# Kernel tuning notes

Hardware: AMD Instinct MI355X
Metric: run time of the kernel (lower is better)

## Reference

```python
import jax, jax.numpy as jnp
import numpy as np

TOP_K = 2
EPS = float(np.finfo(np.float64).eps)  # combine() clamps zeros to np.finfo(float).eps


def setup_inputs() -> dict:
    key = jax.random.key(0)
    ks = jax.random.split(key, 6)
    B, D, H, O, E = 2048, 1024, 2048, 512, 8
    return {
        "x": jax.random.normal(ks[0], (B, D), dtype=jnp.float32),
        "w_gate": jax.random.normal(ks[1], (D, E), dtype=jnp.float32) * 0.02,
        "fc1_w": jax.random.normal(ks[2], (E, D, H), dtype=jnp.float32) * 0.02,
        "fc1_b": jax.random.normal(ks[3], (E, H), dtype=jnp.float32) * 0.02,
        "fc2_w": jax.random.normal(ks[4], (E, H, O), dtype=jnp.float32) * 0.02,
        "fc2_b": jax.random.normal(ks[5], (E, O), dtype=jnp.float32) * 0.02,
    }


def _gates(x, w_gate):
    # Noisy top-k gating in eval mode (no noise): clean logits -> top-k -> softmax over top-k -> scatter.
    logits = x @ w_gate                              # [B, E]
    top_logits, top_idx = jax.lax.top_k(logits, TOP_K)  # [B, K]
    top_gates = jax.nn.softmax(top_logits, axis=-1)      # 'softmax' gating over selected experts
    B = x.shape[0]
    gates = jnp.zeros(logits.shape, logits.dtype)
    gates = gates.at[jnp.arange(B)[:, None], top_idx].set(top_gates)
    return gates                                      # [B, E], zero for non-selected experts


def reference(x, w_gate, fc1_w, fc1_b, fc2_w, fc2_b):
    gates = _gates(x, w_gate)                         # [B, E]
    # Dense-equivalent of SparseDispatcher: non-selected experts have gate 0,
    # so weighting by gates reproduces dispatch/expert/combine exactly.
    h = jax.nn.gelu(jnp.einsum('bd,edh->ebh', x, fc1_w) + fc1_b[:, None, :],
                    approximate=False)                # [E, B, H]
    logp = jax.nn.log_softmax(jnp.einsum('ebh,eho->ebo', h, fc2_w) + fc2_b[:, None, :],
                              axis=-1)                # [E, B, O] (MLP ends with LogSoftmax)
    # combine: sum_e gates[b,e] * exp(logp_e[b]), clamp zeros to eps, then log
    combined = jnp.einsum('ebo,be->bo', jnp.exp(logp), gates)  # [B, O]
    combined = jnp.where(combined == 0, jnp.asarray(EPS, combined.dtype), combined)
    return jnp.log(combined)
```

## Files before the change

kernel.cpp:

```cpp
#include <hip/hip_runtime.h>
#include <stdint.h>

#define Bn 2048
#define Dn 1024
#define Hn 2048
#define On 512
#define En 8

typedef __bf16 bf16x8 __attribute__((ext_vector_type(8)));
typedef float f32x4 __attribute__((ext_vector_type(4)));
typedef unsigned short ushort_t;
typedef ushort_t ushort4v __attribute__((ext_vector_type(4)));

__device__ __forceinline__ ushort_t f2bf(float v) {
  union { float f; uint32_t u; } a; a.f = v;
  uint32_t u = a.u;
  return (ushort_t)((u + 0x7fffu + ((u >> 16) & 1u)) >> 16);
}

__device__ __forceinline__ void gload16(const void* g, void* l) {
  __builtin_amdgcn_global_load_lds((const uint32_t*)g, (uint32_t*)l, 16, 0, 0);
}

__global__ void init_kernel(int* counts, int* cursors) {
  int t = threadIdx.x;
  if (t < En) { counts[t] = 0; cursors[t] = 0; }
}

#define NB_G (Bn / 8)
#define NB_T1 ((Dn / 64) * (Hn / 64) * En)
#define NB_T2 ((Hn / 64) * (On / 64) * En)

__device__ __forceinline__ void tcast64(const float* __restrict__ inp, ushort_t* __restrict__ outp,
                                        int R, int C, int r0, int c0, float* tile ) {
  int t = threadIdx.x;
  int rr = t >> 4;
  int cc4 = (t & 15) * 4;
#pragma unroll
  for (int j = 0; j < 4; j++) {
    float4 v = *(const float4*)&inp[(size_t)(r0 + j * 16 + rr) * C + c0 + cc4];
    float* tp = &tile[(j * 16 + rr) * 65 + cc4];
    tp[0] = v.x; tp[1] = v.y; tp[2] = v.z; tp[3] = v.w;
  }
  __syncthreads();
#pragma unroll
  for (int j = 0; j < 4; j++) {
    int c = j * 16 + rr;
    ushort4v o;
    o[0] = f2bf(tile[(cc4 + 0) * 65 + c]);
    o[1] = f2bf(tile[(cc4 + 1) * 65 + c]);
    o[2] = f2bf(tile[(cc4 + 2) * 65 + c]);
    o[3] = f2bf(tile[(cc4 + 3) * 65 + c]);
    *(ushort4v*)&outp[(size_t)(c0 + c) * R + r0 + cc4] = o;
  }
}

__global__ __launch_bounds__(256) void prep_kernel(
    const float* __restrict__ x, const float* __restrict__ wg,
    const float* __restrict__ fc1w, const float* __restrict__ fc2w,
    ushort_t* __restrict__ x_bf, ushort_t* __restrict__ w1t, ushort_t* __restrict__ w2t,
    int* __restrict__ top_idx, float* __restrict__ gates, int* __restrict__ counts) {
  __shared__ float smem[En * Dn];
  __shared__ int lcnt[En];
  int bid = blockIdx.x;
  int t = threadIdx.x;

  if (bid < NB_G) {
    float* wgs = smem;
    for (int i = t; i < Dn * En; i += 256) {
      int d = i >> 3, e = i & 7;
      wgs[e * Dn + d] = wg[i];
    }
    if (t < En) lcnt[t] = 0;
    __syncthreads();
    int w = t >> 6, lane = t & 63;
#pragma unroll
    for (int r = 0; r < 2; r++) {
      int b = bid * 8 + w * 2 + r;
      const float* xr = x + (size_t)b * Dn;
      ushort_t* xo = x_bf + (size_t)b * Dn;
      float xv[16];
#pragma unroll
      for (int j = 0; j < 16; j++) xv[j] = xr[lane + j * 64];
      float acc[En];
#pragma unroll
      for (int e = 0; e < En; e++) acc[e] = 0.f;
#pragma unroll
      for (int j = 0; j < 16; j++) {
        int d = lane + j * 64;
        xo[d] = f2bf(xv[j]);
#pragma unroll
        for (int e = 0; e < En; e++) acc[e] += xv[j] * wgs[e * Dn + d];
      }
#pragma unroll
      for (int off = 32; off; off >>= 1) {
#pragma unroll
        for (int e = 0; e < En; e++) acc[e] += __shfl_down(acc[e], off);
      }
      if (lane == 0) {
        float best = -1e30f, second = -1e30f; int bi = 0, si = 0;
#pragma unroll
        for (int e = 0; e < En; e++) {
          float l = acc[e];
          if (l > best) { second = best; si = bi; best = l; bi = e; }
          else if (l > second) { second = l; si = e; }
        }
        float e1 = expf(second - best);
        float inv = 1.f / (1.f + e1);
        top_idx[2 * b] = bi; top_idx[2 * b + 1] = si;
        gates[2 * b] = inv;  gates[2 * b + 1] = e1 * inv;
        atomicAdd(&lcnt[bi], 1);
        atomicAdd(&lcnt[si], 1);
      }
    }
    __syncthreads();
    if (t < En) {
      int c = lcnt[t];
      if (c) atomicAdd(&counts[t], c);
    }
  } else if (bid < NB_G + NB_T1) {
    int idx = bid - NB_G;
    constexpr int TPE = (Dn / 64) * (Hn / 64);
    int z = idx / TPE, rem = idx % TPE;
    int r0 = (rem / (Hn / 64)) * 64, c0 = (rem % (Hn / 64)) * 64;
    tcast64(fc1w + (size_t)z * Dn * Hn, w1t + (size_t)z * Dn * Hn, Dn, Hn, r0, c0, smem);
  } else {
    int idx = bid - NB_G - NB_T1;
    constexpr int TPE = (Hn / 64) * (On / 64);
    int z = idx / TPE, rem = idx % TPE;
    int r0 = (rem / (On / 64)) * 64, c0 = (rem % (On / 64)) * 64;
    tcast64(fc2w + (size_t)z * Hn * On, w2t + (size_t)z * Hn * On, Hn, On, r0, c0, smem);
  }
}

__global__ void offsets_kernel(const int* counts, int* offsets, int* cursors) {
  if (threadIdx.x == 0) {
    int s = 0;
    for (int e = 0; e < En; e++) { offsets[e] = s; s += counts[e]; }
  }
  if (threadIdx.x < En) cursors[threadIdx.x] = 0;
}

__global__ void assign_kernel(const int* __restrict__ top_idx, const int* __restrict__ offsets,
                              int* cursors, int* __restrict__ s2r, int* __restrict__ r2s) {
  int b = blockIdx.x * 256 + threadIdx.x;
  if (b >= Bn) return;
#pragma unroll
  for (int k = 0; k < 2; k++) {
    int e = top_idx[2 * b + k];
    int pos = atomicAdd(&cursors[e], 1);
    int slot = offsets[e] + pos;
    s2r[slot] = b;
    r2s[2 * b + k] = slot;
  }
}

template <bool GATHER, bool FC1, int N, int K, int SPLITK>
__global__ __launch_bounds__(256, 8) void moe_gemm_kernel(
    const ushort_t* __restrict__ A, const ushort_t* __restrict__ WT,
    const float* __restrict__ bias, const int* __restrict__ offsets,
    const int* __restrict__ counts, const int* __restrict__ s2r,
    ushort_t* __restrict__ outH, float* __restrict__ outL, float* __restrict__ outL2) {
  constexpr int NBL = N / 64;
  constexpr int KS = K / SPLITK;
  constexpr int NT = KS / 64;
  int e = blockIdx.z;
  int cnt = counts[e];
  int rb = blockIdx.y;
  if (rb * 64 >= cnt) return;
  int base = offsets[e];
  int ks = blockIdx.x / NBL;
  int nb = (blockIdx.x % NBL) * 64;
  int k0 = ks * KS;
  __shared__ __align__(16) ushort_t As[64 * 64];
  __shared__ __align__(16) ushort_t Bs[64 * 64];
  int t = threadIdx.x;
  int lane = t & 63, w = t >> 6;
  int wr = w >> 1, wc = w & 1;

  int srow = t >> 3;
  int scol = ((t & 7) ^ (srow & 7)) * 8;

  const ushort_t* aptr[2];
#pragma unroll
  for (int i = 0; i < 2; i++) {
    int lr = rb * 64 + i * 32 + srow;
    int lrc = lr < cnt ? lr : cnt - 1;
    int slot = base + lrc;
    int row = GATHER ? s2r[slot] : slot;
    aptr[i] = A + (size_t)row * K + k0 + scol;
  }
  const ushort_t* bptr = WT + ((size_t)e * N + nb + srow) * K + k0 + scol;

  f32x4 zero = {0.f, 0.f, 0.f, 0.f};
  f32x4 acc[2][2];
#pragma unroll
  for (int m = 0; m < 2; m++)
#pragma unroll
    for (int n = 0; n < 2; n++) acc[m][n] = zero;

  int a_r = wr * 32 + (lane & 15);
  int b_r = wc * 32 + (lane & 15);
  int axor = lane & 7;
  int c16 = lane >> 4;

  for (int kt = 0; kt < NT; kt++) {
#pragma unroll
    for (int i = 0; i < 2; i++) gload16(aptr[i] + kt * 64, &As[i * 2048 + t * 8]);
#pragma unroll
    for (int i = 0; i < 2; i++)
      gload16(bptr + (size_t)i * 32 * K + kt * 64, &Bs[i * 2048 + t * 8]);
    __syncthreads();
#pragma unroll
    for (int kk = 0; kk < 2; kk++) {
      bf16x8 af[2], bfr[2];
#pragma unroll
      for (int m = 0; m < 2; m++)
        af[m] = *(const bf16x8*)((const char*)As + (a_r + m * 16) * 128 +
                                 (((kk * 4 + c16) ^ axor) << 4));
#pragma unroll
      for (int n = 0; n < 2; n++)
        bfr[n] = *(const bf16x8*)((const char*)Bs + (b_r + n * 16) * 128 +
                                  (((kk * 4 + c16) ^ axor) << 4));
#pragma unroll
      for (int m = 0; m < 2; m++)
#pragma unroll
        for (int n = 0; n < 2; n++)
          acc[m][n] = __builtin_amdgcn_mfma_f32_16x16x32_bf16(af[m], bfr[n], acc[m][n], 0, 0, 0);
    }
    __syncthreads();
  }

  float* dst = (SPLITK > 1 && ks > 0) ? (outL2 + (size_t)(ks - 1) * (2 * Bn * On)) : outL;
  int lr0 = rb * 64 + wr * 32;
#pragma unroll
  for (int m = 0; m < 2; m++) {
#pragma unroll
    for (int i = 0; i < 4; i++) {
      int lr = lr0 + m * 16 + (lane >> 4) * 4 + i;
      if (lr < cnt) {
        int slot = base + lr;
#pragma unroll
        for (int n = 0; n < 2; n++) {
          int col = nb + wc * 32 + n * 16 + (lane & 15);
          float v = acc[m][n][i] + (ks == 0 ? bias[e * N + col] : 0.f);
          if (FC1) {
            float g = 0.5f * v * (1.0f + erff(v * 0.70710678118654752f));
            outH[(size_t)slot * N + col] = f2bf(g);
          } else {
            dst[(size_t)slot * N + col] = v;
          }
        }
      }
    }
  }
}

__device__ __forceinline__ float blk_reduce(float v, bool ismax) {
  __shared__ float sbuf[4];
  int lane = threadIdx.x & 63, w = threadIdx.x >> 6;
#pragma unroll
  for (int off = 32; off; off >>= 1) {
    float o = __shfl_down(v, off);
    v = ismax ? fmaxf(v, o) : (v + o);
  }
  __syncthreads();
  if (lane == 0) sbuf[w] = v;
  __syncthreads();
  float r = sbuf[0];
#pragma unroll
  for (int i = 1; i < 4; i++) r = ismax ? fmaxf(r, sbuf[i]) : (r + sbuf[i]);
  return r;
}

__global__ void combine_kernel(const float* __restrict__ l2a, const float* __restrict__ l2b,
                               const int* __restrict__ r2s, const float* __restrict__ gates,
                               float* __restrict__ out) {
  int b = blockIdx.x, t = threadIdx.x;
  float c0 = 0.f, c1 = 0.f;
#pragma unroll
  for (int k = 0; k < 2; k++) {
    int slot = r2s[2 * b + k];
    float g = gates[2 * b + k];
    const float* lp0 = l2a + (size_t)slot * On;
    float v0 = lp0[t], v1 = lp0[t + 256];
#pragma unroll
    for (int p = 0; p < 3; p++) {
      const float* lpp = l2b + (size_t)p * (2 * Bn * On) + (size_t)slot * On;
      v0 += lpp[t];
      v1 += lpp[t + 256];
    }
    float m = blk_reduce(fmaxf(v0, v1), true);
    float s = blk_reduce(expf(v0 - m) + expf(v1 - m), false);
    float lse = m + logf(s);
    c0 += g * expf(v0 - lse);
    c1 += g * expf(v1 - lse);
  }
  const float EPSv = 2.220446049250313e-16f;
  out[(size_t)b * On + t] = logf(fmaxf(c0, EPSv));
  out[(size_t)b * On + t + 256] = logf(fmaxf(c1, EPSv));
}

extern "C" void kernel_launch(void* const* d_in, const int* in_sizes, int n_in,
                              void* d_out, int out_size, void* d_ws, size_t ws_size,
                              hipStream_t stream) {
  const float* x = (const float*)d_in[0];
  const float* wgate = (const float*)d_in[1];
  const float* fc1w = (const float*)d_in[2];
  const float* fc1b = (const float*)d_in[3];
  const float* fc2w = (const float*)d_in[4];
  const float* fc2b = (const float*)d_in[5];
  float* out = (float*)d_out;

  char* ws = (char*)d_ws;
  size_t o = 0;
  ushort_t* x_bf = (ushort_t*)(ws + o); o += (size_t)Bn * Dn * 2;
  ushort_t* w1t  = (ushort_t*)(ws + o); o += (size_t)En * Hn * Dn * 2;
  ushort_t* w2t  = (ushort_t*)(ws + o); o += (size_t)En * On * Hn * 2;
  ushort_t* hbuf = (ushort_t*)(ws + o); o += (size_t)2 * Bn * Hn * 2;
  float* l2buf   = (float*)(ws + o);    o += (size_t)2 * Bn * On * 4;
  int* top_idx   = (int*)(ws + o);      o += (size_t)Bn * 2 * 4;
  float* gates   = (float*)(ws + o);    o += (size_t)Bn * 2 * 4;
  int* r2s       = (int*)(ws + o);      o += (size_t)Bn * 2 * 4;
  int* s2r       = (int*)(ws + o);      o += (size_t)2 * Bn * 4;
  int* counts    = (int*)(ws + o);      o += 64;
  int* offsets   = (int*)(ws + o);      o += 64;
  int* cursors   = (int*)(ws + o);      o += 64;
  float* l2buf1  = (float*)w1t;

  hipLaunchKernelGGL(init_kernel, dim3(1), dim3(64), 0, stream, counts, cursors);
  hipLaunchKernelGGL(prep_kernel, dim3(NB_G + NB_T1 + NB_T2), dim3(256), 0, stream,
                     x, wgate, fc1w, fc2w, x_bf, w1t, w2t, top_idx, gates, counts);
  hipLaunchKernelGGL(offsets_kernel, dim3(1), dim3(64), 0, stream, counts, offsets, cursors);
  hipLaunchKernelGGL(assign_kernel, dim3(Bn / 256), dim3(256), 0, stream,
                     top_idx, offsets, cursors, s2r, r2s);
  hipLaunchKernelGGL((moe_gemm_kernel<true, true, Hn, Dn, 1>), dim3(Hn / 64, 32, En), dim3(256),
                     0, stream, x_bf, w1t, fc1b, offsets, counts, s2r, hbuf, (float*)nullptr,
                     (float*)nullptr);
  hipLaunchKernelGGL((moe_gemm_kernel<false, false, On, Hn, 4>), dim3((On / 64) * 4, 32, En),
                     dim3(256), 0, stream, hbuf, w2t, fc2b, offsets, counts, s2r,
                     (ushort_t*)nullptr, l2buf, l2buf1);
  hipLaunchKernelGGL(combine_kernel, dim3(Bn), dim3(256), 0, stream, l2buf, l2buf1, r2s, gates, out);
}
```

Baseline: 130.1 us.

## Restructure MoE GEMM to single-wave 64x64 tiles with direct A register loads

Each GEMM block becomes one 64-thread wave that computes the full 64x64 output tile with a 4x4 MFMA accumulator grid, replacing four waves that each held a 2x2 grid. A fragments are now read straight from global memory into registers, so only B is staged through LDS, and the __syncthreads barriers give way to explicit waitcnt and sched_barrier. This is meant to cut LDS traffic and block-level synchronisation and to give each wave more MFMA work per load. The cost is uncoalesced per-lane global reads for A, more registers per thread, and fewer waves per block to hide memory latency.

After: 168.9 us. +29.8%, slower.

```diff
diff --git a/kernel.cpp b/kernel.cpp
--- a/kernel.cpp
+++ b/kernel.cpp
@@ -156,7 +156,7 @@
 }
 
 template <bool GATHER, bool FC1, int N, int K, int SPLITK>
-__global__ __launch_bounds__(256, 8) void moe_gemm_kernel(
+__global__ __launch_bounds__(64, 4) void moe_gemm_kernel(
     const ushort_t* __restrict__ A, const ushort_t* __restrict__ WT,
     const float* __restrict__ bias, const int* __restrict__ offsets,
     const int* __restrict__ counts, const int* __restrict__ s2r,
@@ -172,77 +172,86 @@
   int ks = blockIdx.x / NBL;
   int nb = (blockIdx.x % NBL) * 64;
   int k0 = ks * KS;
-  __shared__ __align__(16) ushort_t As[64 * 64];
   __shared__ __align__(16) ushort_t Bs[64 * 64];
-  int t = threadIdx.x;
-  int lane = t & 63, w = t >> 6;
-  int wr = w >> 1, wc = w & 1;
-
-  int srow = t >> 3;
-  int scol = ((t & 7) ^ (srow & 7)) * 8;
-
-  const ushort_t* aptr[2];
-#pragma unroll
-  for (int i = 0; i < 2; i++) {
-    int lr = rb * 64 + i * 32 + srow;
+  int lane = threadIdx.x;
+
+  int scol = ((lane & 7) ^ (lane >> 3)) * 8;
+  const ushort_t* bptr = WT + ((size_t)e * N + nb + (lane >> 3)) * K + k0 + scol;
+
+  int kg = (lane >> 4) * 8;
+  const ushort_t* aP[4];
+#pragma unroll
+  for (int m = 0; m < 4; m++) {
+    int lr = rb * 64 + m * 16 + (lane & 15);
     int lrc = lr < cnt ? lr : cnt - 1;
     int slot = base + lrc;
     int row = GATHER ? s2r[slot] : slot;
-    aptr[i] = A + (size_t)row * K + k0 + scol;
-  }
-  const ushort_t* bptr = WT + ((size_t)e * N + nb + srow) * K + k0 + scol;
+    aP[m] = A + (size_t)row * K + k0 + kg;
+  }
 
   f32x4 zero = {0.f, 0.f, 0.f, 0.f};
-  f32x4 acc[2][2];
-#pragma unroll
-  for (int m = 0; m < 2; m++)
-#pragma unroll
-    for (int n = 0; n < 2; n++) acc[m][n] = zero;
-
-  int a_r = wr * 32 + (lane & 15);
-  int b_r = wc * 32 + (lane & 15);
+  f32x4 acc[4][4];
+#pragma unroll
+  for (int m = 0; m < 4; m++)
+#pragma unroll
+    for (int n = 0; n < 4; n++) acc[m][n] = zero;
+
+  int b_r = lane & 15;
   int axor = lane & 7;
   int c16 = lane >> 4;
 
   for (int kt = 0; kt < NT; kt++) {
 #pragma unroll
-    for (int i = 0; i < 2; i++) gload16(aptr[i] + kt * 64, &As[i * 2048 + t * 8]);
-#pragma unroll
-    for (int i = 0; i < 2; i++)
-      gload16(bptr + (size_t)i * 32 * K + kt * 64, &Bs[i * 2048 + t * 8]);
-    __syncthreads();
-#pragma unroll
-    for (int kk = 0; kk < 2; kk++) {
-      bf16x8 af[2], bfr[2];
-#pragma unroll
-      for (int m = 0; m < 2; m++)
-        af[m] = *(const bf16x8*)((const char*)As + (a_r + m * 16) * 128 +
-                                 (((kk * 4 + c16) ^ axor) << 4));
-#pragma unroll
-      for (int n = 0; n < 2; n++)
+    for (int i = 0; i < 8; i++)
+      gload16(bptr + (size_t)i * 8 * K + kt * 64, &Bs[i * 512 + lane * 8]);
+    bf16x8 af0[4];
+#pragma unroll
+    for (int m = 0; m < 4; m++) af0[m] = *(const bf16x8*)(aP[m] + kt * 64);
+    asm volatile("s_waitcnt vmcnt(0)" ::: "memory");
+    __builtin_amdgcn_sched_barrier(0);
+    bf16x8 af1[4];
+#pragma unroll
+    for (int m = 0; m < 4; m++) af1[m] = *(const bf16x8*)(aP[m] + kt * 64 + 32);
+    {
+      bf16x8 bfr[4];
+#pragma unroll
+      for (int n = 0; n < 4; n++)
         bfr[n] = *(const bf16x8*)((const char*)Bs + (b_r + n * 16) * 128 +
-                                  (((kk * 4 + c16) ^ axor) << 4));
-#pragma unroll
-      for (int m = 0; m < 2; m++)
-#pragma unroll
-        for (int n = 0; n < 2; n++)
-          acc[m][n] = __builtin_amdgcn_mfma_f32_16x16x32_bf16(af[m], bfr[n], acc[m][n], 0, 0, 0);
-    }
-    __syncthreads();
+                                  ((c16 ^ axor) << 4));
+#pragma unroll
+      for (int m = 0; m < 4; m++)
+#pragma unroll
+        for (int n = 0; n < 4; n++)
+          acc[m][n] = __builtin_amdgcn_mfma_f32_16x16x32_bf16(af0[m], bfr[n], acc[m][n], 0, 0, 0);
+    }
+    {
+      bf16x8 bfr[4];
+#pragma unroll
+      for (int n = 0; n < 4; n++)
+        bfr[n] = *(const bf16x8*)((const char*)Bs + (b_r + n * 16) * 128 +
+                                  (((4 + c16) ^ axor) << 4));
+#pragma unroll
+      for (int m = 0; m < 4; m++)
+#pragma unroll
+        for (int n = 0; n < 4; n++)
+          acc[m][n] = __builtin_amdgcn_mfma_f32_16x16x32_bf16(af1[m], bfr[n], acc[m][n], 0, 0, 0);
+    }
+    asm volatile("s_waitcnt lgkmcnt(0)" ::: "memory");
+    __builtin_amdgcn_sched_barrier(0);
   }
 
   float* dst = (SPLITK > 1 && ks > 0) ? (outL2 + (size_t)(ks - 1) * (2 * Bn * On)) : outL;
-  int lr0 = rb * 64 + wr * 32;
-#pragma unroll
-  for (int m = 0; m < 2; m++) {
+  int lr0 = rb * 64;
+#pragma unroll
+  for (int m = 0; m < 4; m++) {
 #pragma unroll
     for (int i = 0; i < 4; i++) {
       int lr = lr0 + m * 16 + (lane >> 4) * 4 + i;
       if (lr < cnt) {
         int slot = base + lr;
 #pragma unroll
-        for (int n = 0; n < 2; n++) {
-          int col = nb + wc * 32 + n * 16 + (lane & 15);
+        for (int n = 0; n < 4; n++) {
+          int col = nb + n * 16 + (lane & 15);
           float v = acc[m][n][i] + (ks == 0 ? bias[e * N + col] : 0.f);
           if (FC1) {
             float g = 0.5f * v * (1.0f + erff(v * 0.70710678118654752f));
@@ -334,11 +343,11 @@
   hipLaunchKernelGGL(offsets_kernel, dim3(1), dim3(64), 0, stream, counts, offsets, cursors);
   hipLaunchKernelGGL(assign_kernel, dim3(Bn / 256), dim3(256), 0, stream,
                      top_idx, offsets, cursors, s2r, r2s);
-  hipLaunchKernelGGL((moe_gemm_kernel<true, true, Hn, Dn, 1>), dim3(Hn / 64, 32, En), dim3(256),
+  hipLaunchKernelGGL((moe_gemm_kernel<true, true, Hn, Dn, 1>), dim3(Hn / 64, 32, En), dim3(64),
                      0, stream, x_bf, w1t, fc1b, offsets, counts, s2r, hbuf, (float*)nullptr,
                      (float*)nullptr);
   hipLaunchKernelGGL((moe_gemm_kernel<false, false, On, Hn, 4>), dim3((On / 64) * 4, 32, En),
-                     dim3(256), 0, stream, hbuf, w2t, fc2b, offsets, counts, s2r,
+                     dim3(64), 0, stream, hbuf, w2t, fc2b, offsets, counts, s2r,
                      (ushort_t*)nullptr, l2buf, l2buf1);
   hipLaunchKernelGGL(combine_kernel, dim3(Bn), dim3(256), 0, stream, l2buf, l2buf1, r2s, gates, out);
 }
```

## Widen MoE GEMM block tiles to 64x256 and 64x128 with per-wave 64-row strips

Applied to the files above, without the earlier changes.

Reorganizes the MoE GEMM tiling so each wave computes all 64 rows across a WCOLS-wide column strip, making the block tile 64x256 for fc1 and 64x128 for fc2. This reuses each A tile across more output columns, which cuts redundant A loads and gather traffic and raises MFMA count per LDS read. Launch bounds drop to 2 blocks per CU to allow more accumulator registers. The cost is fewer blocks, which may reduce parallelism for experts with few tokens, plus larger LDS use.

New measurement: 137.5 us. +5.6%, slower.

```diff
diff --git a/kernel.cpp b/kernel.cpp
--- a/kernel.cpp
+++ b/kernel.cpp
@@ -155,13 +155,15 @@
   }
 }
 
-template <bool GATHER, bool FC1, int N, int K, int SPLITK>
-__global__ __launch_bounds__(256, 8) void moe_gemm_kernel(
+template <bool GATHER, bool FC1, int N, int K, int SPLITK, int WCOLS>
+__global__ __launch_bounds__(256, 2) void moe_gemm_kernel(
     const ushort_t* __restrict__ A, const ushort_t* __restrict__ WT,
     const float* __restrict__ bias, const int* __restrict__ offsets,
     const int* __restrict__ counts, const int* __restrict__ s2r,
     ushort_t* __restrict__ outH, float* __restrict__ outL, float* __restrict__ outL2) {
-  constexpr int NBL = N / 64;
+  constexpr int BCOLS = 4 * WCOLS;
+  constexpr int WC16 = WCOLS / 16;
+  constexpr int NBL = N / BCOLS;
   constexpr int KS = K / SPLITK;
   constexpr int NT = KS / 64;
   int e = blockIdx.z;
@@ -170,13 +172,12 @@
   if (rb * 64 >= cnt) return;
   int base = offsets[e];
   int ks = blockIdx.x / NBL;
-  int nb = (blockIdx.x % NBL) * 64;
+  int nb = (blockIdx.x % NBL) * BCOLS;
   int k0 = ks * KS;
   __shared__ __align__(16) ushort_t As[64 * 64];
-  __shared__ __align__(16) ushort_t Bs[64 * 64];
+  __shared__ __align__(16) ushort_t Bs[BCOLS * 64];
   int t = threadIdx.x;
   int lane = t & 63, w = t >> 6;
-  int wr = w >> 1, wc = w & 1;
 
   int srow = t >> 3;
   int scol = ((t & 7) ^ (srow & 7)) * 8;
@@ -193,14 +194,14 @@
   const ushort_t* bptr = WT + ((size_t)e * N + nb + srow) * K + k0 + scol;
 
   f32x4 zero = {0.f, 0.f, 0.f, 0.f};
-  f32x4 acc[2][2];
-#pragma unroll
-  for (int m = 0; m < 2; m++)
-#pragma unroll
-    for (int n = 0; n < 2; n++) acc[m][n] = zero;
-
-  int a_r = wr * 32 + (lane & 15);
-  int b_r = wc * 32 + (lane & 15);
+  f32x4 acc[4][WC16];
+#pragma unroll
+  for (int m = 0; m < 4; m++)
+#pragma unroll
+    for (int n = 0; n < WC16; n++) acc[m][n] = zero;
+
+  int a_r = lane & 15;
+  int b_r = w * WCOLS + (lane & 15);
   int axor = lane & 7;
   int c16 = lane >> 4;
 
@@ -208,41 +209,41 @@
 #pragma unroll
     for (int i = 0; i < 2; i++) gload16(aptr[i] + kt * 64, &As[i * 2048 + t * 8]);
 #pragma unroll
-    for (int i = 0; i < 2; i++)
+    for (int i = 0; i < WCOLS / 8; i++)
       gload16(bptr + (size_t)i * 32 * K + kt * 64, &Bs[i * 2048 + t * 8]);
     __syncthreads();
 #pragma unroll
     for (int kk = 0; kk < 2; kk++) {
-      bf16x8 af[2], bfr[2];
-#pragma unroll
-      for (int m = 0; m < 2; m++)
+      bf16x8 af[4], bfr[WC16];
+#pragma unroll
+      for (int m = 0; m < 4; m++)
         af[m] = *(const bf16x8*)((const char*)As + (a_r + m * 16) * 128 +
                                  (((kk * 4 + c16) ^ axor) << 4));
 #pragma unroll
-      for (int n = 0; n < 2; n++)
+      for (int n = 0; n < WC16; n++)
         bfr[n] = *(const bf16x8*)((const char*)Bs + (b_r + n * 16) * 128 +
                                   (((kk * 4 + c16) ^ axor) << 4));
 #pragma unroll
-      for (int m = 0; m < 2; m++)
-#pragma unroll
-        for (int n = 0; n < 2; n++)
+      for (int m = 0; m < 4; m++)
+#pragma unroll
+        for (int n = 0; n < WC16; n++)
           acc[m][n] = __builtin_amdgcn_mfma_f32_16x16x32_bf16(af[m], bfr[n], acc[m][n], 0, 0, 0);
     }
     __syncthreads();
   }
 
   float* dst = (SPLITK > 1 && ks > 0) ? (outL2 + (size_t)(ks - 1) * (2 * Bn * On)) : outL;
-  int lr0 = rb * 64 + wr * 32;
-#pragma unroll
-  for (int m = 0; m < 2; m++) {
+  int lr0 = rb * 64;
+#pragma unroll
+  for (int m = 0; m < 4; m++) {
 #pragma unroll
     for (int i = 0; i < 4; i++) {
       int lr = lr0 + m * 16 + (lane >> 4) * 4 + i;
       if (lr < cnt) {
         int slot = base + lr;
 #pragma unroll
-        for (int n = 0; n < 2; n++) {
-          int col = nb + wc * 32 + n * 16 + (lane & 15);
+        for (int n = 0; n < WC16; n++) {
+          int col = nb + w * WCOLS + n * 16 + (lane & 15);
           float v = acc[m][n][i] + (ks == 0 ? bias[e * N + col] : 0.f);
           if (FC1) {
             float g = 0.5f * v * (1.0f + erff(v * 0.70710678118654752f));
@@ -334,10 +335,10 @@
   hipLaunchKernelGGL(offsets_kernel, dim3(1), dim3(64), 0, stream, counts, offsets, cursors);
   hipLaunchKernelGGL(assign_kernel, dim3(Bn / 256), dim3(256), 0, stream,
                      top_idx, offsets, cursors, s2r, r2s);
-  hipLaunchKernelGGL((moe_gemm_kernel<true, true, Hn, Dn, 1>), dim3(Hn / 64, 32, En), dim3(256),
-                     0, stream, x_bf, w1t, fc1b, offsets, counts, s2r, hbuf, (float*)nullptr,
-                     (float*)nullptr);
-  hipLaunchKernelGGL((moe_gemm_kernel<false, false, On, Hn, 4>), dim3((On / 64) * 4, 32, En),
+  hipLaunchKernelGGL((moe_gemm_kernel<true, true, Hn, Dn, 1, 64>), dim3(Hn / 256, 32, En),
+                     dim3(256), 0, stream, x_bf, w1t, fc1b, offsets, counts, s2r, hbuf,
+                     (float*)nullptr, (float*)nullptr);
+  hipLaunchKernelGGL((moe_gemm_kernel<false, false, On, Hn, 4, 32>), dim3((On / 128) * 4, 32, En),
                      dim3(256), 0, stream, hbuf, w2t, fc2b, offsets, counts, s2r,
                      (ushort_t*)nullptr, l2buf, l2buf1);
   hipLaunchKernelGGL(combine_kernel, dim3(Bn), dim3(256), 0, stream, l2buf, l2buf1, r2s, gates, out);
```
